# Kernel tuning notes

Measured on AMD Instinct MI355X. Metric: run time of the kernel, lower is better.

The kernel has to match this reference:

```python
import jax, jax.numpy as jnp
import numpy as np

B, S, D, H, KD = 4, 2048, 640, 10, 64


def setup_inputs() -> dict:
    key = jax.random.key(0)
    k0, k1, k2, k3, k4 = jax.random.split(key, 5)
    x = jax.random.normal(k0, (B, S, D), dtype=jnp.float32)
    # per-head projection weights, stacked over heads: [H, D, KD]
    Wq = jax.random.normal(k1, (H, D, KD), dtype=jnp.float32) * 0.05
    Wk = jax.random.normal(k2, (H, D, KD), dtype=jnp.float32) * 0.05
    Wv = jax.random.normal(k3, (H, D, KD), dtype=jnp.float32) * 0.05
    # output projection: [H*KD, D]
    Wo = jax.random.normal(k4, (H * KD, D), dtype=jnp.float32) * 0.05
    return {"x": x, "Wq": Wq, "Wk": Wk, "Wv": Wv, "Wo": Wo}


def reference(x, Wq, Wk, Wv, Wo):
    # Batched equivalent of the per-head Python loop:
    # each head computes q=x@Wq_h, k=x@Wk_h, v=x@Wv_h, softmax(q k^T / sqrt(KD)) @ v
    q = jnp.einsum("bsd,hdk->bhsk", x, Wq)
    k = jnp.einsum("bsd,hdk->bhsk", x, Wk)
    v = jnp.einsum("bsd,hdk->bhsk", x, Wv)
    scale = 1.0 / jnp.sqrt(jnp.asarray(KD, x.dtype))
    scores = jnp.einsum("bhsk,bhtk->bhst", q, k) * scale  # [B,H,S,S]
    attn = jax.nn.softmax(scores, axis=-1)
    z = jnp.einsum("bhst,bhtk->bhsk", attn, v)  # [B,H,S,KD]
    # concat heads along last axis (head 0 first, matching the loop order)
    z = z.transpose(0, 2, 1, 3).reshape(x.shape[0], x.shape[1], H * KD)
    return jnp.einsum("bsf,fd->bsd", z, Wo)
```

## Files before the change

### kernel.cpp

```cpp
#include <hip/hip_runtime.h>
#include <hip/hip_bf16.h>

#define B_  4
#define S_  2048
#define D_  640
#define H_  10
#define KD_ 64

typedef __attribute__((ext_vector_type(8))) short  short8;
typedef __attribute__((ext_vector_type(4))) short  short4v;
typedef __attribute__((ext_vector_type(4))) float  floatx4;
typedef __attribute__((ext_vector_type(2))) unsigned int uint2v;

static __device__ __forceinline__ short f2bf_fast(float f) {
    unsigned int u = __float_as_uint(f);
    u += 0x7fffu + ((u >> 16) & 1u);
    return (short)(u >> 16);
}
static __device__ __forceinline__ unsigned int pack2bf(float a, float b) {
    union { __hip_bfloat162 h; unsigned int u; } c;
    c.h = __float22bfloat162_rn(float2{a, b});
    return c.u;
}

static __device__ __forceinline__ void gload_lds16(const void* gp, void* lp) {
    __builtin_amdgcn_global_load_lds(
        (const __attribute__((address_space(1))) unsigned int*)gp,
        (__attribute__((address_space(3))) unsigned int*)lp, 16, 0, 0);
}

__global__ __launch_bounds__(256) void prep(
        const float* __restrict__ x,
        const float* __restrict__ Wq, const float* __restrict__ Wk,
        const float* __restrict__ Wv, const float* __restrict__ Wo,
        short* __restrict__ xb, short* __restrict__ BigT,
        short* __restrict__ WoT) {
    __shared__ float tile[32][33];
    int bid = blockIdx.x;
    if (bid < 5120) {
        int idx = (bid * 256 + threadIdx.x) * 4;
        float4 v = *(const float4*)(x + idx);
        uint2v o;
        o[0] = pack2bf(v.x, v.y);
        o[1] = pack2bf(v.z, v.w);
        *(uint2v*)(xb + idx) = o;
    } else if (bid < 6320) {
        int flat = bid - 5120;
        int bz = flat / 40, rem = flat % 40;
        int by = rem >> 1, bxx = rem & 1;
        int w = bz / 10, h = bz % 10;
        const float* W = ((w == 0) ? Wq : (w == 1) ? Wk : Wv) + h * 640 * 64;
        short* out = BigT + (w * 640 + h * 64) * 640;
        int c0 = bxx * 32;
        int r0 = by * 32;
        int tx = threadIdx.x & 31, ty = threadIdx.x >> 5;
        #pragma unroll
        for (int k = 0; k < 4; ++k)
            tile[ty + 8 * k][tx] = W[(r0 + ty + 8 * k) * 64 + c0 + tx];
        __syncthreads();
        #pragma unroll
        for (int k = 0; k < 4; ++k)
            out[(c0 + ty + 8 * k) * 640 + r0 + tx] = f2bf_fast(tile[tx][ty + 8 * k]);
    } else {
        int flat = bid - 6320;
        int c0 = (flat % 20) * 32;
        int r0 = (flat / 20) * 32;
        int tx = threadIdx.x & 31, ty = threadIdx.x >> 5;
        #pragma unroll
        for (int k = 0; k < 4; ++k)
            tile[ty + 8 * k][tx] = Wo[(r0 + ty + 8 * k) * 640 + c0 + tx];
        __syncthreads();
        #pragma unroll
        for (int k = 0; k < 4; ++k)
            WoT[(c0 + ty + 8 * k) * 640 + r0 + tx] = f2bf_fast(tile[tx][ty + 8 * k]);
    }
}


__global__ __launch_bounds__(256) void qkv_gemm(
        const short* __restrict__ X, const short* __restrict__ BigT,
        short* __restrict__ qb, short* __restrict__ kb, short* __restrict__ vtb) {
    __shared__ __align__(16) short Ab[2][128][32];
    __shared__ __align__(16) short Bb[2][128][32];

    int wave = threadIdx.x >> 6;
    int lane = threadIdx.x & 63;
    int lq = lane & 15, quad = lane >> 4;
    int wm = (wave & 1) * 64, wn = (wave >> 1) * 64;
    int tm = blockIdx.x * 128;
    int tn = blockIdx.y * 128;

    int srow = lane >> 2;
    int schunk = (lane & 3) ^ ((lane >> 3) & 3);
    const short* Asrc0 = X    + (tm + wave * 32 + srow) * 640 + schunk * 8;
    const short* Bsrc0 = BigT + (tn + wave * 32 + srow) * 640 + schunk * 8;
    const short* Asrc1 = Asrc0 + 16 * 640;
    const short* Bsrc1 = Bsrc0 + 16 * 640;

    floatx4 acc[4][4];
    for (int a = 0; a < 4; ++a)
        for (int n = 0; n < 4; ++n)
            acc[a][n] = (floatx4){0.f, 0.f, 0.f, 0.f};

    int rsw = (lq >> 1) & 3;

    gload_lds16(Asrc0, &Ab[0][wave * 32][0]);
    gload_lds16(Asrc1, &Ab[0][wave * 32 + 16][0]);
    gload_lds16(Bsrc0, &Bb[0][wave * 32][0]);
    gload_lds16(Bsrc1, &Bb[0][wave * 32 + 16][0]);

    int p = 0;
    bool isV = (tn >= 1280);

    for (int k0 = 0; k0 < 640; k0 += 32) {
        __syncthreads();
        if (k0 + 32 < 640) {
            int pn = p ^ 1;
            gload_lds16(Asrc0 + k0 + 32, &Ab[pn][wave * 32][0]);
            gload_lds16(Asrc1 + k0 + 32, &Ab[pn][wave * 32 + 16][0]);
            gload_lds16(Bsrc0 + k0 + 32, &Bb[pn][wave * 32][0]);
            gload_lds16(Bsrc1 + k0 + 32, &Bb[pn][wave * 32 + 16][0]);
        }

        short8 af[4], bf[4];
        #pragma unroll
        for (int t = 0; t < 4; ++t) {
            af[t] = *(const short8*)(&Ab[p][wm + t * 16 + lq][(quad ^ rsw) * 8]);
            bf[t] = *(const short8*)(&Bb[p][wn + t * 16 + lq][(quad ^ rsw) * 8]);
        }
        if (!isV) {
            #pragma unroll
            for (int mt = 0; mt < 4; ++mt)
                #pragma unroll
                for (int nt = 0; nt < 4; ++nt)
                    acc[mt][nt] = __builtin_amdgcn_mfma_f32_16x16x32_bf16(
                        af[mt], bf[nt], acc[mt][nt], 0, 0, 0);
        } else {
            #pragma unroll
            for (int nt = 0; nt < 4; ++nt)
                #pragma unroll
                for (int mt = 0; mt < 4; ++mt)
                    acc[nt][mt] = __builtin_amdgcn_mfma_f32_16x16x32_bf16(
                        bf[nt], af[mt], acc[nt][mt], 0, 0, 0);
        }
        p ^= 1;
    }

    if (!isV) {
        const float qscale = 0.18033688011112042f;
        short* dst = (tn < 640) ? qb : kb;
        float scale = (tn < 640) ? qscale : 1.0f;
        #pragma unroll
        for (int nt = 0; nt < 4; ++nt) {
            int rem = (tn + wn + nt * 16) % 640;
            int hh = rem / 64, kd = (rem % 64) + lq;
            #pragma unroll
            for (int mt = 0; mt < 4; ++mt) {
                #pragma unroll
                for (int r = 0; r < 4; ++r) {
                    int m = tm + wm + mt * 16 + quad * 4 + r;
                    int b = m >> 11, s = m & 2047;
                    dst[((b * H_ + hh) * S_ + s) * KD_ + kd] =
                        f2bf_fast(acc[mt][nt][r] * scale);
                }
            }
        }
    } else {
        #pragma unroll
        for (int nt = 0; nt < 4; ++nt) {
            int rem = (tn + wn + nt * 16) - 1280;
            int hh = rem / 64;
            int kd0 = (rem % 64) + quad * 4;
            #pragma unroll
            for (int mt = 0; mt < 4; ++mt) {
                int m = tm + wm + mt * 16 + lq;
                int b = m >> 11, s = m & 2047;
                #pragma unroll
                for (int r = 0; r < 4; ++r) {
                    vtb[((b * H_ + hh) * KD_ + kd0 + r) * S_ + s] =
                        f2bf_fast(acc[nt][mt][r]);
                }
            }
        }
    }
}

__global__ __launch_bounds__(256, 3) void attn(
        const short* __restrict__ qb, const short* __restrict__ kbuf,
        const short* __restrict__ vtb, short* __restrict__ zb) {
    __shared__ __align__(16) short Kbuf[2][64][64];
    __shared__ __align__(16) short Vbuf[2][64][64];
    __shared__ __align__(16) short Pbuf[4][2][16][72];

    int wave = threadIdx.x >> 6;
    int lane = threadIdx.x & 63;
    int lq = lane & 15, quad = lane >> 4;

    int bx = blockIdx.x;
    int xcd = bx & 7, slot = bx >> 3;
    int bh = xcd * 5 + (slot >> 4);
    int qt = slot & 15;
    int b = bh / 10, h = bh % 10;
    int q0 = qt * 128;

    const short* qp = qb + (b * H_ + h) * S_ * KD_;
    const short* kp = kbuf + (b * H_ + h) * S_ * KD_;
    const short* vp = vtb + (b * H_ + h) * KD_ * S_;

    int r8 = lane >> 3;
    int g  = (lane & 7) ^ r8;
    const short* kg0 = kp + (wave * 16 + r8) * 64 + g * 8;
    const short* kg1 = kp + (wave * 16 + 8 + r8) * 64 + g * 8;
    const short* vg0 = vp + (wave * 16 + r8) * (long)S_ + g * 8;
    const short* vg1 = vp + (wave * 16 + 8 + r8) * (long)S_ + g * 8;

    short8 qA0, qA1, qB0, qB1;
    {
        int rowA = q0 + wave * 32 + lq;
        qA0 = *(const short8*)(qp + rowA * 64 + quad * 8);
        qA1 = *(const short8*)(qp + rowA * 64 + 32 + quad * 8);
        qB0 = *(const short8*)(qp + (rowA + 16) * 64 + quad * 8);
        qB1 = *(const short8*)(qp + (rowA + 16) * 64 + 32 + quad * 8);
    }

    short8 ones;
    #pragma unroll
    for (int i = 0; i < 8; ++i) ones[i] = (short)0x3F80;

    floatx4 OA[4], OB[4];
    for (int n = 0; n < 4; ++n) {
        OA[n] = (floatx4){0.f, 0.f, 0.f, 0.f};
        OB[n] = (floatx4){0.f, 0.f, 0.f, 0.f};
    }
    floatx4 lsvA = (floatx4){0.f, 0.f, 0.f, 0.f};
    floatx4 lsvB = (floatx4){0.f, 0.f, 0.f, 0.f};

    gload_lds16(kg0, &Kbuf[0][wave * 16][0]);
    gload_lds16(kg1, &Kbuf[0][wave * 16 + 8][0]);
    gload_lds16(vg0, &Vbuf[0][wave * 16][0]);
    gload_lds16(vg1, &Vbuf[0][wave * 16 + 8][0]);

    int p = 0;
    int sw = lq & 7;

    for (int t0 = 0; t0 < S_; t0 += 64) {
        __syncthreads();

        if (t0 + 64 < S_) {
            int pn = p ^ 1;
            gload_lds16(kg0 + (t0 + 64) * 64, &Kbuf[pn][wave * 16][0]);
            gload_lds16(kg1 + (t0 + 64) * 64, &Kbuf[pn][wave * 16 + 8][0]);
            gload_lds16(vg0 + (t0 + 64),      &Vbuf[pn][wave * 16][0]);
            gload_lds16(vg1 + (t0 + 64),      &Vbuf[pn][wave * 16 + 8][0]);
        }

        const short* Kb = &Kbuf[p][0][0];
        const short* Vb = &Vbuf[p][0][0];

        floatx4 sTA[4], sTB[4];
        #pragma unroll
        for (int kblk = 0; kblk < 4; ++kblk) {
            const short* krow = Kb + (kblk * 16 + lq) * 64;
            short8 bk0 = *(const short8*)(krow + (quad ^ sw) * 8);
            short8 bk1 = *(const short8*)(krow + ((quad + 4) ^ sw) * 8);
            floatx4 zA = (floatx4){0.f, 0.f, 0.f, 0.f};
            zA = __builtin_amdgcn_mfma_f32_16x16x32_bf16(bk0, qA0, zA, 0, 0, 0);
            sTA[kblk] = __builtin_amdgcn_mfma_f32_16x16x32_bf16(bk1, qA1, zA, 0, 0, 0);
            floatx4 zB = (floatx4){0.f, 0.f, 0.f, 0.f};
            zB = __builtin_amdgcn_mfma_f32_16x16x32_bf16(bk0, qB0, zB, 0, 0, 0);
            sTB[kblk] = __builtin_amdgcn_mfma_f32_16x16x32_bf16(bk1, qB1, zB, 0, 0, 0);
        }

        #pragma unroll
        for (int kblk = 0; kblk < 4; ++kblk) {
            uint2v wa;
            wa[0] = pack2bf(__builtin_amdgcn_exp2f(sTA[kblk][0]),
                            __builtin_amdgcn_exp2f(sTA[kblk][1]));
            wa[1] = pack2bf(__builtin_amdgcn_exp2f(sTA[kblk][2]),
                            __builtin_amdgcn_exp2f(sTA[kblk][3]));
            *(uint2v*)(&Pbuf[wave][0][lq][kblk * 16 + quad * 4]) = wa;
            uint2v wb;
            wb[0] = pack2bf(__builtin_amdgcn_exp2f(sTB[kblk][0]),
                            __builtin_amdgcn_exp2f(sTB[kblk][1]));
            wb[1] = pack2bf(__builtin_amdgcn_exp2f(sTB[kblk][2]),
                            __builtin_amdgcn_exp2f(sTB[kblk][3]));
            *(uint2v*)(&Pbuf[wave][1][lq][kblk * 16 + quad * 4]) = wb;
        }

        #pragma unroll
        for (int ts = 0; ts < 2; ++ts) {
            short8 pfA = *(const short8*)(&Pbuf[wave][0][lq][ts * 32 + quad * 8]);
            short8 pfB = *(const short8*)(&Pbuf[wave][1][lq][ts * 32 + quad * 8]);
            lsvA = __builtin_amdgcn_mfma_f32_16x16x32_bf16(ones, pfA, lsvA, 0, 0, 0);
            lsvB = __builtin_amdgcn_mfma_f32_16x16x32_bf16(ones, pfB, lsvB, 0, 0, 0);
            #pragma unroll
            for (int db = 0; db < 4; ++db) {
                const short* vrow = Vb + (db * 16 + lq) * 64;
                short8 bv = *(const short8*)(vrow + ((ts * 4 + quad) ^ sw) * 8);
                OA[db] = __builtin_amdgcn_mfma_f32_16x16x32_bf16(bv, pfA, OA[db], 0, 0, 0);
                OB[db] = __builtin_amdgcn_mfma_f32_16x16x32_bf16(bv, pfB, OB[db], 0, 0, 0);
            }
        }

        p ^= 1;
    }

    float invA = 1.0f / lsvA[0];
    float invB = 1.0f / lsvB[0];

    int sA = q0 + wave * 32 + lq;
    int sB = sA + 16;
    short* zrA = zb + (b * S_ + sA) * 640 + h * 64;
    short* zrB = zb + (b * S_ + sB) * 640 + h * 64;
    #pragma unroll
    for (int db = 0; db < 4; ++db) {
        uint2v za, zv;
        za[0] = pack2bf(OA[db][0] * invA, OA[db][1] * invA);
        za[1] = pack2bf(OA[db][2] * invA, OA[db][3] * invA);
        *(uint2v*)(zrA + db * 16 + quad * 4) = za;
        zv[0] = pack2bf(OB[db][0] * invB, OB[db][1] * invB);
        zv[1] = pack2bf(OB[db][2] * invB, OB[db][3] * invB);
        *(uint2v*)(zrB + db * 16 + quad * 4) = zv;
    }
}

__global__ __launch_bounds__(256) void out_gemm(
        const short* __restrict__ Z, const short* __restrict__ WoT,
        float* __restrict__ out) {
    __shared__ __align__(16) short Ab[2][128][32];
    __shared__ __align__(16) short Bb[2][128][32];

    int wave = threadIdx.x >> 6;
    int lane = threadIdx.x & 63;
    int lq = lane & 15, quad = lane >> 4;
    int wm = (wave & 1) * 64, wn = (wave >> 1) * 64;
    int tm = blockIdx.x * 128;
    int tn = blockIdx.y * 128;

    int srow = lane >> 2;
    int schunk = (lane & 3) ^ ((lane >> 3) & 3);
    const short* Asrc0 = Z   + (tm + wave * 32 + srow) * 640 + schunk * 8;
    const short* Bsrc0 = WoT + (tn + wave * 32 + srow) * 640 + schunk * 8;
    const short* Asrc1 = Asrc0 + 16 * 640;
    const short* Bsrc1 = Bsrc0 + 16 * 640;

    floatx4 acc[4][4];
    for (int a = 0; a < 4; ++a)
        for (int n = 0; n < 4; ++n)
            acc[a][n] = (floatx4){0.f, 0.f, 0.f, 0.f};

    int rsw = (lq >> 1) & 3;

    gload_lds16(Asrc0, &Ab[0][wave * 32][0]);
    gload_lds16(Asrc1, &Ab[0][wave * 32 + 16][0]);
    gload_lds16(Bsrc0, &Bb[0][wave * 32][0]);
    gload_lds16(Bsrc1, &Bb[0][wave * 32 + 16][0]);

    int p = 0;
    for (int k0 = 0; k0 < 640; k0 += 32) {
        __syncthreads();
        if (k0 + 32 < 640) {
            int pn = p ^ 1;
            gload_lds16(Asrc0 + k0 + 32, &Ab[pn][wave * 32][0]);
            gload_lds16(Asrc1 + k0 + 32, &Ab[pn][wave * 32 + 16][0]);
            gload_lds16(Bsrc0 + k0 + 32, &Bb[pn][wave * 32][0]);
            gload_lds16(Bsrc1 + k0 + 32, &Bb[pn][wave * 32 + 16][0]);
        }

        short8 af[4], bf[4];
        #pragma unroll
        for (int t = 0; t < 4; ++t) {
            af[t] = *(const short8*)(&Ab[p][wm + t * 16 + lq][(quad ^ rsw) * 8]);
            bf[t] = *(const short8*)(&Bb[p][wn + t * 16 + lq][(quad ^ rsw) * 8]);
        }
        #pragma unroll
        for (int mt = 0; mt < 4; ++mt)
            #pragma unroll
            for (int nt = 0; nt < 4; ++nt)
                acc[mt][nt] = __builtin_amdgcn_mfma_f32_16x16x32_bf16(
                    af[mt], bf[nt], acc[mt][nt], 0, 0, 0);
        p ^= 1;
    }

    #pragma unroll
    for (int mt = 0; mt < 4; ++mt) {
        #pragma unroll
        for (int nt = 0; nt < 4; ++nt) {
            #pragma unroll
            for (int r = 0; r < 4; ++r) {
                int m = tm + wm + mt * 16 + quad * 4 + r;
                out[m * 640 + tn + wn + nt * 16 + lq] = acc[mt][nt][r];
            }
        }
    }
}

extern "C" void kernel_launch(void* const* d_in, const int* in_sizes, int n_in,
                              void* d_out, int out_size, void* d_ws, size_t ws_size,
                              hipStream_t stream) {
    const float* x  = (const float*)d_in[0];
    const float* Wq = (const float*)d_in[1];
    const float* Wk = (const float*)d_in[2];
    const float* Wv = (const float*)d_in[3];
    const float* Wo = (const float*)d_in[4];
    float* out = (float*)d_out;

    char* ws = (char*)d_ws;
    short* BigT = (short*)(ws);
    short* WoT  = (short*)(ws + 2457600);
    short* xb   = (short*)(ws + 3276800);
    short* qb   = (short*)(ws + 13762560);
    short* kb   = (short*)(ws + 24248320);
    short* vtb  = (short*)(ws + 34734080);
    short* zb   = (short*)(ws + 45219840);

    prep<<<dim3(6720), dim3(256), 0, stream>>>(x, Wq, Wk, Wv, Wo, xb, BigT, WoT);
    qkv_gemm<<<dim3(64, 15), dim3(256), 0, stream>>>(xb, BigT, qb, kb, vtb);
    attn<<<dim3(640), dim3(256), 0, stream>>>(qb, kb, vtb, zb);
    out_gemm<<<dim3(64, 5), dim3(256), 0, stream>>>(zb, WoT, out);
}
```

Measured before the change: 194.0 us.

## Use permlane swaps instead of LDS for P fragments and halve attention tile

The attention kernel now builds the bf16 probability fragment for the PV MFMA in registers with permlane32/permlane16 swaps, dropping the per-wave LDS P buffer round trip. Each wave now processes 16 query rows instead of 32, so blocks cover 64 queries. The grid doubles to 1280 blocks and the launch bounds allow 6 blocks per CU. This trades K/V reuse per block (K/V tiles are loaded twice as often overall) for lower register/LDS pressure, more occupancy and no LDS writes or reads for P.

```diff
diff --git a/kernel.cpp b/kernel.cpp
--- a/kernel.cpp
+++ b/kernel.cpp
@@ -185,12 +185,11 @@
     }
 }
 
-__global__ __launch_bounds__(256, 3) void attn(
+__global__ __launch_bounds__(256, 6) void attn(
         const short* __restrict__ qb, const short* __restrict__ kbuf,
         const short* __restrict__ vtb, short* __restrict__ zb) {
     __shared__ __align__(16) short Kbuf[2][64][64];
     __shared__ __align__(16) short Vbuf[2][64][64];
-    __shared__ __align__(16) short Pbuf[4][2][16][72];
 
     int wave = threadIdx.x >> 6;
     int lane = threadIdx.x & 63;
@@ -198,10 +197,10 @@
 
     int bx = blockIdx.x;
     int xcd = bx & 7, slot = bx >> 3;
-    int bh = xcd * 5 + (slot >> 4);
-    int qt = slot & 15;
+    int bh = xcd * 5 + (slot >> 5);
+    int qt = slot & 31;
     int b = bh / 10, h = bh % 10;
-    int q0 = qt * 128;
+    int q0 = qt * 64;
 
     const short* qp = qb + (b * H_ + h) * S_ * KD_;
     const short* kp = kbuf + (b * H_ + h) * S_ * KD_;
@@ -214,26 +213,21 @@
     const short* vg0 = vp + (wave * 16 + r8) * (long)S_ + g * 8;
     const short* vg1 = vp + (wave * 16 + 8 + r8) * (long)S_ + g * 8;
 
-    short8 qA0, qA1, qB0, qB1;
+    short8 qA0, qA1;
     {
-        int rowA = q0 + wave * 32 + lq;
+        int rowA = q0 + wave * 16 + lq;
         qA0 = *(const short8*)(qp + rowA * 64 + quad * 8);
         qA1 = *(const short8*)(qp + rowA * 64 + 32 + quad * 8);
-        qB0 = *(const short8*)(qp + (rowA + 16) * 64 + quad * 8);
-        qB1 = *(const short8*)(qp + (rowA + 16) * 64 + 32 + quad * 8);
     }
 
     short8 ones;
     #pragma unroll
     for (int i = 0; i < 8; ++i) ones[i] = (short)0x3F80;
 
-    floatx4 OA[4], OB[4];
-    for (int n = 0; n < 4; ++n) {
+    floatx4 OA[4];
+    for (int n = 0; n < 4; ++n)
         OA[n] = (floatx4){0.f, 0.f, 0.f, 0.f};
-        OB[n] = (floatx4){0.f, 0.f, 0.f, 0.f};
-    }
     floatx4 lsvA = (floatx4){0.f, 0.f, 0.f, 0.f};
-    floatx4 lsvB = (floatx4){0.f, 0.f, 0.f, 0.f};
 
     gload_lds16(kg0, &Kbuf[0][wave * 16][0]);
     gload_lds16(kg1, &Kbuf[0][wave * 16 + 8][0]);
@@ -257,48 +251,45 @@
         const short* Kb = &Kbuf[p][0][0];
         const short* Vb = &Vbuf[p][0][0];
 
-        floatx4 sTA[4], sTB[4];
+        floatx4 sT[4];
         #pragma unroll
         for (int kblk = 0; kblk < 4; ++kblk) {
             const short* krow = Kb + (kblk * 16 + lq) * 64;
             short8 bk0 = *(const short8*)(krow + (quad ^ sw) * 8);
             short8 bk1 = *(const short8*)(krow + ((quad + 4) ^ sw) * 8);
-            floatx4 zA = (floatx4){0.f, 0.f, 0.f, 0.f};
-            zA = __builtin_amdgcn_mfma_f32_16x16x32_bf16(bk0, qA0, zA, 0, 0, 0);
-            sTA[kblk] = __builtin_amdgcn_mfma_f32_16x16x32_bf16(bk1, qA1, zA, 0, 0, 0);
-            floatx4 zB = (floatx4){0.f, 0.f, 0.f, 0.f};
-            zB = __builtin_amdgcn_mfma_f32_16x16x32_bf16(bk0, qB0, zB, 0, 0, 0);
-            sTB[kblk] = __builtin_amdgcn_mfma_f32_16x16x32_bf16(bk1, qB1, zB, 0, 0, 0);
-        }
-
-        #pragma unroll
-        for (int kblk = 0; kblk < 4; ++kblk) {
-            uint2v wa;
-            wa[0] = pack2bf(__builtin_amdgcn_exp2f(sTA[kblk][0]),
-                            __builtin_amdgcn_exp2f(sTA[kblk][1]));
-            wa[1] = pack2bf(__builtin_amdgcn_exp2f(sTA[kblk][2]),
-                            __builtin_amdgcn_exp2f(sTA[kblk][3]));
-            *(uint2v*)(&Pbuf[wave][0][lq][kblk * 16 + quad * 4]) = wa;
-            uint2v wb;
-            wb[0] = pack2bf(__builtin_amdgcn_exp2f(sTB[kblk][0]),
-                            __builtin_amdgcn_exp2f(sTB[kblk][1]));
-            wb[1] = pack2bf(__builtin_amdgcn_exp2f(sTB[kblk][2]),
-                            __builtin_amdgcn_exp2f(sTB[kblk][3]));
-            *(uint2v*)(&Pbuf[wave][1][lq][kblk * 16 + quad * 4]) = wb;
+            floatx4 z = (floatx4){0.f, 0.f, 0.f, 0.f};
+            z = __builtin_amdgcn_mfma_f32_16x16x32_bf16(bk0, qA0, z, 0, 0, 0);
+            sT[kblk] = __builtin_amdgcn_mfma_f32_16x16x32_bf16(bk1, qA1, z, 0, 0, 0);
         }
 
         #pragma unroll
         for (int ts = 0; ts < 2; ++ts) {
-            short8 pfA = *(const short8*)(&Pbuf[wave][0][lq][ts * 32 + quad * 8]);
-            short8 pfB = *(const short8*)(&Pbuf[wave][1][lq][ts * 32 + quad * 8]);
-            lsvA = __builtin_amdgcn_mfma_f32_16x16x32_bf16(ones, pfA, lsvA, 0, 0, 0);
-            lsvB = __builtin_amdgcn_mfma_f32_16x16x32_bf16(ones, pfB, lsvB, 0, 0, 0);
+            int ka = ts * 2, kc = ts * 2 + 1;
+            unsigned int c00 = pack2bf(__builtin_amdgcn_exp2f(sT[ka][0]),
+                                       __builtin_amdgcn_exp2f(sT[ka][1]));
+            unsigned int c01 = pack2bf(__builtin_amdgcn_exp2f(sT[ka][2]),
+                                       __builtin_amdgcn_exp2f(sT[ka][3]));
+            unsigned int c10 = pack2bf(__builtin_amdgcn_exp2f(sT[kc][0]),
+                                       __builtin_amdgcn_exp2f(sT[kc][1]));
+            unsigned int c11 = pack2bf(__builtin_amdgcn_exp2f(sT[kc][2]),
+                                       __builtin_amdgcn_exp2f(sT[kc][3]));
+            uint2v s0 = __builtin_amdgcn_permlane32_swap(c00, c10, false, false);
+            uint2v s1 = __builtin_amdgcn_permlane32_swap(c01, c11, false, false);
+            uint2v w02 = __builtin_amdgcn_permlane16_swap(s0[0], s0[1], false, false);
+            uint2v w13 = __builtin_amdgcn_permlane16_swap(s1[0], s1[1], false, false);
+            union { unsigned int u[4]; short8 s8; } pfu;
+            pfu.u[0] = w02[0];
+            pfu.u[1] = w13[0];
+            pfu.u[2] = w02[1];
+            pfu.u[3] = w13[1];
+            short8 pf = pfu.s8;
+
+            lsvA = __builtin_amdgcn_mfma_f32_16x16x32_bf16(ones, pf, lsvA, 0, 0, 0);
             #pragma unroll
             for (int db = 0; db < 4; ++db) {
                 const short* vrow = Vb + (db * 16 + lq) * 64;
                 short8 bv = *(const short8*)(vrow + ((ts * 4 + quad) ^ sw) * 8);
-                OA[db] = __builtin_amdgcn_mfma_f32_16x16x32_bf16(bv, pfA, OA[db], 0, 0, 0);
-                OB[db] = __builtin_amdgcn_mfma_f32_16x16x32_bf16(bv, pfB, OB[db], 0, 0, 0);
+                OA[db] = __builtin_amdgcn_mfma_f32_16x16x32_bf16(bv, pf, OA[db], 0, 0, 0);
             }
         }
 
@@ -306,21 +297,15 @@
     }
 
     float invA = 1.0f / lsvA[0];
-    float invB = 1.0f / lsvB[0];
-
-    int sA = q0 + wave * 32 + lq;
-    int sB = sA + 16;
+
+    int sA = q0 + wave * 16 + lq;
     short* zrA = zb + (b * S_ + sA) * 640 + h * 64;
-    short* zrB = zb + (b * S_ + sB) * 640 + h * 64;
     #pragma unroll
     for (int db = 0; db < 4; ++db) {
-        uint2v za, zv;
+        uint2v za;
         za[0] = pack2bf(OA[db][0] * invA, OA[db][1] * invA);
         za[1] = pack2bf(OA[db][2] * invA, OA[db][3] * invA);
         *(uint2v*)(zrA + db * 16 + quad * 4) = za;
-        zv[0] = pack2bf(OB[db][0] * invB, OB[db][1] * invB);
-        zv[1] = pack2bf(OB[db][2] * invB, OB[db][3] * invB);
-        *(uint2v*)(zrB + db * 16 + quad * 4) = zv;
     }
 }
 
@@ -416,6 +401,6 @@
 
     prep<<<dim3(6720), dim3(256), 0, stream>>>(x, Wq, Wk, Wv, Wo, xb, BigT, WoT);
     qkv_gemm<<<dim3(64, 15), dim3(256), 0, stream>>>(xb, BigT, qb, kb, vtb);
-    attn<<<dim3(640), dim3(256), 0, stream>>>(qb, kb, vtb, zb);
+    attn<<<dim3(1280), dim3(256), 0, stream>>>(qb, kb, vtb, zb);
     out_gemm<<<dim3(64, 5), dim3(256), 0, stream>>>(zb, WoT, out);
 }
```

Result: slower. 201.8 us (+4.0%).

## Redistribute softmax probabilities via permlane swaps instead of LDS round-trip

Applied to the files above, without the earlier changes.

The exponentiated score tiles no longer go through a per-wave shared-memory buffer to be rearranged into the MFMA operand layout. Instead, permlane32_swap and permlane16_swap shuffle the packed bf16 values directly between lanes in registers. This removes the LDS writes and reads and frees shared memory, which could raise occupancy. The MFMA sections are also wrapped in s_setprio so waves issuing matrix work get scheduling priority, at the cost of a few extra instructions and added register pressure.

```diff
diff --git a/kernel.cpp b/kernel.cpp
--- a/kernel.cpp
+++ b/kernel.cpp
@@ -190,7 +190,6 @@
         const short* __restrict__ vtb, short* __restrict__ zb) {
     __shared__ __align__(16) short Kbuf[2][64][64];
     __shared__ __align__(16) short Vbuf[2][64][64];
-    __shared__ __align__(16) short Pbuf[4][2][16][72];
 
     int wave = threadIdx.x >> 6;
     int lane = threadIdx.x & 63;
@@ -258,6 +257,7 @@
         const short* Vb = &Vbuf[p][0][0];
 
         floatx4 sTA[4], sTB[4];
+        __builtin_amdgcn_s_setprio(1);
         #pragma unroll
         for (int kblk = 0; kblk < 4; ++kblk) {
             const short* krow = Kb + (kblk * 16 + lq) * 64;
@@ -270,27 +270,49 @@
             zB = __builtin_amdgcn_mfma_f32_16x16x32_bf16(bk0, qB0, zB, 0, 0, 0);
             sTB[kblk] = __builtin_amdgcn_mfma_f32_16x16x32_bf16(bk1, qB1, zB, 0, 0, 0);
         }
-
-        #pragma unroll
-        for (int kblk = 0; kblk < 4; ++kblk) {
-            uint2v wa;
-            wa[0] = pack2bf(__builtin_amdgcn_exp2f(sTA[kblk][0]),
-                            __builtin_amdgcn_exp2f(sTA[kblk][1]));
-            wa[1] = pack2bf(__builtin_amdgcn_exp2f(sTA[kblk][2]),
-                            __builtin_amdgcn_exp2f(sTA[kblk][3]));
-            *(uint2v*)(&Pbuf[wave][0][lq][kblk * 16 + quad * 4]) = wa;
-            uint2v wb;
-            wb[0] = pack2bf(__builtin_amdgcn_exp2f(sTB[kblk][0]),
-                            __builtin_amdgcn_exp2f(sTB[kblk][1]));
-            wb[1] = pack2bf(__builtin_amdgcn_exp2f(sTB[kblk][2]),
-                            __builtin_amdgcn_exp2f(sTB[kblk][3]));
-            *(uint2v*)(&Pbuf[wave][1][lq][kblk * 16 + quad * 4]) = wb;
-        }
+        __builtin_amdgcn_s_setprio(0);
 
         #pragma unroll
         for (int ts = 0; ts < 2; ++ts) {
-            short8 pfA = *(const short8*)(&Pbuf[wave][0][lq][ts * 32 + quad * 8]);
-            short8 pfB = *(const short8*)(&Pbuf[wave][1][lq][ts * 32 + quad * 8]);
+            int ka = ts * 2, kc = ts * 2 + 1;
+            unsigned int a00 = pack2bf(__builtin_amdgcn_exp2f(sTA[ka][0]),
+                                       __builtin_amdgcn_exp2f(sTA[ka][1]));
+            unsigned int a01 = pack2bf(__builtin_amdgcn_exp2f(sTA[ka][2]),
+                                       __builtin_amdgcn_exp2f(sTA[ka][3]));
+            unsigned int a10 = pack2bf(__builtin_amdgcn_exp2f(sTA[kc][0]),
+                                       __builtin_amdgcn_exp2f(sTA[kc][1]));
+            unsigned int a11 = pack2bf(__builtin_amdgcn_exp2f(sTA[kc][2]),
+                                       __builtin_amdgcn_exp2f(sTA[kc][3]));
+            uint2v sa0 = __builtin_amdgcn_permlane32_swap(a00, a10, false, false);
+            uint2v sa1 = __builtin_amdgcn_permlane32_swap(a01, a11, false, false);
+            uint2v wa02 = __builtin_amdgcn_permlane16_swap(sa0[0], sa0[1], false, false);
+            uint2v wa13 = __builtin_amdgcn_permlane16_swap(sa1[0], sa1[1], false, false);
+            union { unsigned int u[4]; short8 s8; } pfa;
+            pfa.u[0] = wa02[0];
+            pfa.u[1] = wa13[0];
+            pfa.u[2] = wa02[1];
+            pfa.u[3] = wa13[1];
+            short8 pfA = pfa.s8;
+            unsigned int b00 = pack2bf(__builtin_amdgcn_exp2f(sTB[ka][0]),
+                                       __builtin_amdgcn_exp2f(sTB[ka][1]));
+            unsigned int b01 = pack2bf(__builtin_amdgcn_exp2f(sTB[ka][2]),
+                                       __builtin_amdgcn_exp2f(sTB[ka][3]));
+            unsigned int b10 = pack2bf(__builtin_amdgcn_exp2f(sTB[kc][0]),
+                                       __builtin_amdgcn_exp2f(sTB[kc][1]));
+            unsigned int b11 = pack2bf(__builtin_amdgcn_exp2f(sTB[kc][2]),
+                                       __builtin_amdgcn_exp2f(sTB[kc][3]));
+            uint2v sb0 = __builtin_amdgcn_permlane32_swap(b00, b10, false, false);
+            uint2v sb1 = __builtin_amdgcn_permlane32_swap(b01, b11, false, false);
+            uint2v wb02 = __builtin_amdgcn_permlane16_swap(sb0[0], sb0[1], false, false);
+            uint2v wb13 = __builtin_amdgcn_permlane16_swap(sb1[0], sb1[1], false, false);
+            union { unsigned int u[4]; short8 s8; } pfb;
+            pfb.u[0] = wb02[0];
+            pfb.u[1] = wb13[0];
+            pfb.u[2] = wb02[1];
+            pfb.u[3] = wb13[1];
+            short8 pfB = pfb.s8;
+
+            __builtin_amdgcn_s_setprio(1);
             lsvA = __builtin_amdgcn_mfma_f32_16x16x32_bf16(ones, pfA, lsvA, 0, 0, 0);
             lsvB = __builtin_amdgcn_mfma_f32_16x16x32_bf16(ones, pfB, lsvB, 0, 0, 0);
             #pragma unroll
@@ -300,6 +322,7 @@
                 OA[db] = __builtin_amdgcn_mfma_f32_16x16x32_bf16(bv, pfA, OA[db], 0, 0, 0);
                 OB[db] = __builtin_amdgcn_mfma_f32_16x16x32_bf16(bv, pfB, OB[db], 0, 0, 0);
             }
+            __builtin_amdgcn_s_setprio(0);
         }
 
         p ^= 1;
```

Result: no change. 191.3 us (-1.4%).
